# Kernel tuning notes

Hardware: AMD Instinct MI355X
Metric: run time of the kernel (lower is better)

Reference implementation:

```python
import jax, jax.numpy as jnp
import numpy as np

B, S, H, NH, HD = 4, 4096, 1024, 16, 64

def setup_inputs() -> dict:
    key = jax.random.key(0)
    ks = jax.random.split(key, 5)
    scale = 1.0 / np.sqrt(H)
    return {
        "hidden_states": jax.random.normal(ks[0], (B, S, H), dtype=jnp.float32),
        "Wq": jax.random.normal(ks[1], (H, H), dtype=jnp.float32) * scale,
        "Wk": jax.random.normal(ks[2], (H, H), dtype=jnp.float32) * scale,
        "Wv": jax.random.normal(ks[3], (H, H), dtype=jnp.float32) * scale,
        "Wo": jax.random.normal(ks[4], (H, H), dtype=jnp.float32) * scale,
    }

def reference(hidden_states, Wq, Wk, Wv, Wo):
    b, s, h = hidden_states.shape
    # torch nn.Linear: y = x @ W.T
    q = (hidden_states @ Wq.T).reshape(b, s, NH, HD)
    k = (hidden_states @ Wk.T).reshape(b, s, NH, HD)
    v = (hidden_states @ Wv.T).reshape(b, s, NH, HD)
    # feature map: ELU (as in source, no +1)
    q = jax.nn.elu(q)
    k = jax.nn.elu(k)
    # per-head kv state: sum over sequence of outer products k_s v_s^T -> [b,h,d,e]
    kv = jnp.einsum('bshd,bshe->bhde', k, v)
    out = jnp.einsum('bqhd,bhde->bqhe', q, kv)  # [b,s,h,e]
    out = out.reshape(b, s, h)
    return out @ Wo.T  # dropout p=0.0 is identity
```

## Files before the change

### kernel.cpp

```cpp
#include <hip/hip_runtime.h>
#include <cstdint>
#include <cstddef>

#define B_  4
#define S_  4096
#define H_  1024
#define NH_ 16
#define M_  (B_*S_)

typedef __bf16 bf16x8 __attribute__((ext_vector_type(8)));
typedef float  f32x4  __attribute__((ext_vector_type(4)));

__device__ __forceinline__ unsigned short f2b(float f) {
  union { float f; unsigned u; } v; v.f = f;
  unsigned r = v.u + 0x7FFFu + ((v.u >> 16) & 1u);
  return (unsigned short)(r >> 16);
}
__device__ __forceinline__ float b2f(unsigned short u) {
  union { unsigned u; float f; } v; v.u = ((unsigned)u) << 16;
  return v.f;
}

#define GLD16(g, l) __builtin_amdgcn_global_load_lds( \
    (const __attribute__((address_space(1))) void*)(g), \
    (__attribute__((address_space(3))) void*)(l), 16, 0, 0)

#define VM0()  asm volatile("s_waitcnt vmcnt(0)" ::: "memory")
#define BAR()  do { asm volatile("" ::: "memory"); __builtin_amdgcn_s_barrier(); \
                    asm volatile("" ::: "memory"); } while (0)

__global__ void cast_f32_bf16(const float* __restrict__ src,
                              unsigned short* __restrict__ dst, int n4) {
  int i = blockIdx.x * blockDim.x + threadIdx.x;
  if (i >= n4) return;
  float4 f = reinterpret_cast<const float4*>(src)[i];
  ushort4 o;
  o.x = f2b(f.x); o.y = f2b(f.y); o.z = f2b(f.z); o.w = f2b(f.w);
  reinterpret_cast<ushort4*>(dst)[i] = o;
}

__global__ void cast_w4(const float* __restrict__ w0, const float* __restrict__ w1,
                        const float* __restrict__ w2, const float* __restrict__ w3,
                        unsigned short* __restrict__ dst) {
  int i = blockIdx.x * blockDim.x + threadIdx.x;
  int w = i >> 18, j = i & 0x3FFFF;
  const float* src = (w == 0) ? w0 : (w == 1) ? w1 : (w == 2) ? w2 : w3;
  float4 f = reinterpret_cast<const float4*>(src)[j];
  ushort4 o;
  o.x = f2b(f.x); o.y = f2b(f.y); o.z = f2b(f.z); o.w = f2b(f.w);
  reinterpret_cast<ushort4*>(dst)[i] = o;
}

template<int MODE>
__global__ __launch_bounds__(512, 2) void gemm256(
    const unsigned short* __restrict__ A_,
    const unsigned short* __restrict__ Bt_,
    void* __restrict__ out) {
  __shared__ __align__(16) unsigned short LDS[2][2][16384];

  const int NTN = (MODE == 0) ? 12 : 4;
  const int nx  = gridDim.x >> 3;
  const int b2  = (blockIdx.x & 7) * nx + (blockIdx.x >> 3);
  const int tileM = (b2 / NTN) << 8;
  const int tileN = (b2 % NTN) << 8;

  const unsigned short* Bt_e =
      (MODE == 1) ? (Bt_ + ((size_t)(tileM >> 12) << 20)) : Bt_;

  const int tid  = threadIdx.x;
  const int lane = tid & 63, wv = tid >> 6;
  const int wmi  = wv >> 2;
  const int wni  = wv & 3;
  const int fr   = lane & 15, fq = lane >> 4;

  const int sr0 = tid >> 3,          sc0 = (tid & 7) ^ (sr0 & 7);
  const int sr1 = (tid + 512) >> 3,  sc1 = (tid & 7) ^ (sr1 & 7);

#define STG(NB, ARR, HM, SRC, RB, TT) do {                                      \
    GLD16((SRC) + (size_t)((RB) + (HM)*128 + sr0) * 1024 + (TT)*64 + sc0*8,     \
          &LDS[NB][ARR][(HM)*8192 + wv*512]);                                   \
    GLD16((SRC) + (size_t)((RB) + (HM)*128 + sr1) * 1024 + (TT)*64 + sc1*8,     \
          &LDS[NB][ARR][(HM)*8192 + 4096 + wv*512]);                            \
  } while (0)

#define LOADA(CB, MQ) do {                                                      \
    _Pragma("unroll")                                                           \
    for (int m = 0; m < 4; m++) {                                               \
      int r = (MQ)*128 + wmi*64 + m*16 + fr;                                    \
      af[m][0] = *(const bf16x8*)&LDS[CB][0][r*64 + ((fq    ) ^ (r&7))*8];      \
      af[m][1] = *(const bf16x8*)&LDS[CB][0][r*64 + ((4 + fq) ^ (r&7))*8];      \
    }                                                                           \
  } while (0)

#define LOADB(CB, NQ) do {                                                      \
    _Pragma("unroll")                                                           \
    for (int n = 0; n < 2; n++) {                                               \
      int r = (NQ)*128 + wni*32 + n*16 + fr;                                    \
      bv[n][0] = *(const bf16x8*)&LDS[CB][1][r*64 + ((fq    ) ^ (r&7))*8];      \
      bv[n][1] = *(const bf16x8*)&LDS[CB][1][r*64 + ((4 + fq) ^ (r&7))*8];      \
    }                                                                           \
  } while (0)

#define MM(MQ, NQ) do {                                                         \
    __builtin_amdgcn_s_setprio(1);                                              \
    _Pragma("unroll")                                                           \
    for (int m = 0; m < 4; m++)                                                 \
      _Pragma("unroll")                                                         \
      for (int n = 0; n < 2; n++) {                                             \
        acc[MQ][NQ][m][n] = __builtin_amdgcn_mfma_f32_16x16x32_bf16(            \
            af[m][0], bv[n][0], acc[MQ][NQ][m][n], 0, 0, 0);                    \
        acc[MQ][NQ][m][n] = __builtin_amdgcn_mfma_f32_16x16x32_bf16(            \
            af[m][1], bv[n][1], acc[MQ][NQ][m][n], 0, 0, 0);                    \
      }                                                                         \
    __builtin_amdgcn_s_setprio(0);                                              \
  } while (0)

  f32x4 zero = {0.f, 0.f, 0.f, 0.f};
  f32x4 acc[2][2][4][2];
#pragma unroll
  for (int a = 0; a < 2; a++)
#pragma unroll
    for (int b = 0; b < 2; b++)
#pragma unroll
      for (int m = 0; m < 4; m++)
#pragma unroll
        for (int n = 0; n < 2; n++) acc[a][b][m][n] = zero;

  bf16x8 af[4][2], bv[2][2];

  STG(0, 0, 0, A_,   tileM, 0);
  STG(0, 0, 1, A_,   tileM, 0);
  STG(0, 1, 0, Bt_e, tileN, 0);
  STG(0, 1, 1, Bt_e, tileN, 0);
  VM0();
  BAR();

  int cb = 0;
  for (int t = 0; t < 15; ++t) {
    const int nb = cb ^ 1;
    LOADA(cb, 0); LOADB(cb, 0);
    STG(nb, 0, 0, A_,   tileM, t + 1);
    STG(nb, 1, 0, Bt_e, tileN, t + 1);
    BAR(); MM(0, 0); BAR();
    LOADB(cb, 1);
    STG(nb, 1, 1, Bt_e, tileN, t + 1);
    BAR(); MM(0, 1); BAR();
    LOADA(cb, 1);
    STG(nb, 0, 1, A_,   tileM, t + 1);
    BAR(); MM(1, 1); BAR();
    LOADB(cb, 0);
    VM0();
    BAR(); MM(1, 0); BAR();
    cb = nb;
  }
  LOADA(cb, 0); LOADB(cb, 0);
  BAR(); MM(0, 0); BAR();
  LOADB(cb, 1);
  BAR(); MM(0, 1); BAR();
  LOADA(cb, 1);
  BAR(); MM(1, 1); BAR();
  LOADB(cb, 0);
  BAR(); MM(1, 0);

#pragma unroll
  for (int mq = 0; mq < 2; mq++)
#pragma unroll
    for (int nq = 0; nq < 2; nq++)
#pragma unroll
      for (int m = 0; m < 4; m++)
#pragma unroll
        for (int n = 0; n < 2; n++)
#pragma unroll
          for (int r = 0; r < 4; r++) {
            int row = tileM + mq * 128 + wmi * 64 + m * 16 + fq * 4 + r;
            int col = tileN + nq * 128 + wni * 32 + n * 16 + fr;
            float v = acc[mq][nq][m][n][r];
            if (MODE == 0) {
              int reg = col >> 10, lc = col & 1023;
              if (reg < 2) v = v > 0.f ? v : (expf(v) - 1.f);
              ((unsigned short*)out)[(size_t)reg * ((size_t)M_ * H_) +
                                     (size_t)row * H_ + lc] = f2b(v);
            } else {
              ((float*)out)[(size_t)row * H_ + col] = v;
            }
          }
#undef MM
#undef LOADB
#undef LOADA
#undef STG
}

__global__ __launch_bounds__(256) void kv_partial(
    const unsigned short* __restrict__ Kb,
    const unsigned short* __restrict__ Vb,
    float* __restrict__ kvp) {
  __shared__ __align__(16) unsigned short kt[32 * 64];
  __shared__ __align__(16) unsigned short vt[32 * 64];
  const int bh = blockIdx.x >> 4;
  const int ch = blockIdx.x & 15;
  const int b  = bh >> 4, h = bh & 15;
  const int t  = threadIdx.x;
  const int rr = t >> 3;
  const int cc = (t & 7) * 8;
  const int d0 = (t >> 4) * 4;
  const int e0 = (t & 15) * 4;

  float acc[4][4] = {};
  for (int s0 = ch * 256; s0 < ch * 256 + 256; s0 += 32) {
    size_t g = (size_t)(b * S_ + s0 + rr) * H_ + h * 64 + cc;
    *reinterpret_cast<uint4*>(&kt[rr * 64 + cc]) = *reinterpret_cast<const uint4*>(Kb + g);
    *reinterpret_cast<uint4*>(&vt[rr * 64 + cc]) = *reinterpret_cast<const uint4*>(Vb + g);
    __syncthreads();
#pragma unroll 4
    for (int ss = 0; ss < 32; ss++) {
      ushort4 k4 = *reinterpret_cast<const ushort4*>(&kt[ss * 64 + d0]);
      ushort4 v4 = *reinterpret_cast<const ushort4*>(&vt[ss * 64 + e0]);
      float kf[4] = {b2f(k4.x), b2f(k4.y), b2f(k4.z), b2f(k4.w)};
      float vf[4] = {b2f(v4.x), b2f(v4.y), b2f(v4.z), b2f(v4.w)};
#pragma unroll
      for (int i = 0; i < 4; i++)
#pragma unroll
        for (int j = 0; j < 4; j++) acc[i][j] += kf[i] * vf[j];
    }
    __syncthreads();
  }
  float* outp = kvp + (size_t)blockIdx.x * 4096;
#pragma unroll
  for (int i = 0; i < 4; i++)
#pragma unroll
    for (int j = 0; j < 4; j++) outp[(d0 + i) * 64 + e0 + j] = acc[i][j];
}

__global__ __launch_bounds__(256) void kv_reduce(
    const float* __restrict__ kvp, unsigned short* __restrict__ KVb) {
  const int bh = blockIdx.x;
#pragma unroll
  for (int i = 0; i < 16; i++) {
    int idx = threadIdx.x + i * 256;
    float s = 0.f;
#pragma unroll
    for (int ch = 0; ch < 16; ch++) s += kvp[(size_t)(bh * 16 + ch) * 4096 + idx];
    KVb[(size_t)bh * 4096 + idx] = f2b(s);
  }
}

__global__ __launch_bounds__(256) void merge_m(
    const unsigned short* __restrict__ KVb,
    const unsigned short* __restrict__ Wob,
    unsigned short* __restrict__ MbT) {
  const int bh = blockIdx.x >> 2;
  const int nc = blockIdx.x & 3;
  const int b  = bh >> 4, h = bh & 15;
  const int lane = threadIdx.x & 63, wv = threadIdx.x >> 6;
  const int fr = lane & 15, fq = lane >> 4;
  const int ncb = nc * 256 + wv * 64;

  f32x4 zero = {0.f, 0.f, 0.f, 0.f};
  f32x4 acc[4][4];
#pragma unroll
  for (int i = 0; i < 4; i++)
#pragma unroll
    for (int j = 0; j < 4; j++) acc[i][j] = zero;

#pragma unroll
  for (int kk = 0; kk < 2; kk++) {
    bf16x8 af[4], bvv[4];
#pragma unroll
    for (int i = 0; i < 4; i++)
      af[i] = *(const bf16x8*)&KVb[(size_t)bh * 4096 + (i * 16 + fr) * 64 + kk * 32 + fq * 8];
#pragma unroll
    for (int j = 0; j < 4; j++)
      bvv[j] = *(const bf16x8*)&Wob[(size_t)(ncb + j * 16 + fr) * 1024 + h * 64 + kk * 32 + fq * 8];
#pragma unroll
    for (int i = 0; i < 4; i++)
#pragma unroll
      for (int j = 0; j < 4; j++)
        acc[i][j] = __builtin_amdgcn_mfma_f32_16x16x32_bf16(af[i], bvv[j], acc[i][j], 0, 0, 0);
  }
#pragma unroll
  for (int i = 0; i < 4; i++)
#pragma unroll
    for (int j = 0; j < 4; j++)
#pragma unroll
      for (int r = 0; r < 4; r++) {
        int n = ncb + j * 16 + fr;
        int k = h * 64 + i * 16 + fq * 4 + r;
        MbT[((size_t)b << 20) + (size_t)n * 1024 + k] = f2b(acc[i][j][r]);
      }
}

extern "C" void kernel_launch(void* const* d_in, const int* in_sizes, int n_in,
                              void* d_out, int out_size, void* d_ws, size_t ws_size,
                              hipStream_t stream) {
  (void)in_sizes; (void)n_in; (void)out_size; (void)ws_size;
  const float* X  = (const float*)d_in[0];
  const float* Wq = (const float*)d_in[1];
  const float* Wk = (const float*)d_in[2];
  const float* Wv = (const float*)d_in[3];
  const float* Wo = (const float*)d_in[4];

  char*  ws  = (char*)d_ws;
  size_t off = 0;
  auto alloc = [&](size_t bytes) -> char* {
    char* p = ws + off;
    off += (bytes + 255) & ~(size_t)255;
    return p;
  };
  unsigned short* Xb   = (unsigned short*)alloc((size_t)M_ * H_ * 2);
  unsigned short* Wcat = (unsigned short*)alloc((size_t)4 * H_ * H_ * 2);
  unsigned short* QKVb = (unsigned short*)alloc((size_t)3 * M_ * H_ * 2);
  float*          kvp  = (float*)alloc((size_t)64 * 16 * 4096 * 4);
  unsigned short* KVb  = (unsigned short*)alloc((size_t)64 * 4096 * 2);
  unsigned short* MbT  = (unsigned short*)alloc((size_t)4 * H_ * H_ * 2);

  unsigned short* Qb = QKVb;
  unsigned short* Kb = QKVb + (size_t)M_ * H_;
  unsigned short* Vb = QKVb + (size_t)2 * M_ * H_;
  unsigned short* Wob = Wcat + (size_t)3 * H_ * H_;

  cast_f32_bf16<<<(M_ * H_) / 1024, 256, 0, stream>>>(X, Xb, (M_ * H_) / 4);
  cast_w4<<<(4 * H_ * H_) / 1024, 256, 0, stream>>>(Wq, Wk, Wv, Wo, Wcat);

  gemm256<0><<<768, 512, 0, stream>>>(Xb, Wcat, QKVb);

  kv_partial<<<1024, 256, 0, stream>>>(Kb, Vb, kvp);
  kv_reduce<<<64, 256, 0, stream>>>(kvp, KVb);
  merge_m<<<256, 256, 0, stream>>>(KVb, Wob, MbT);

  gemm256<1><<<256, 512, 0, stream>>>(Qb, MbT, (float*)d_out);
}
```

Baseline: 276.1 us.

## Stage GEMM epilogue through swizzled LDS for vectorized stores, hoist prefetches

The GEMM epilogue now writes accumulators into swizzled shared memory and then emits 16-byte coalesced global stores, replacing scattered 2-byte and 4-byte stores. All next-tile global-to-LDS prefetches are issued at the start of each k-iteration instead of being interleaved between MMA phases. The KV partial kernel uses 8 sequence chunks instead of 16, which halves the partial buffer and the reduce work. The costs are extra barriers and LDS traffic in the epilogue, and less parallelism in kv_partial.

```diff
diff --git a/kernel.cpp b/kernel.cpp
--- a/kernel.cpp
+++ b/kernel.cpp
@@ -140,13 +140,13 @@
     const int nb = cb ^ 1;
     LOADA(cb, 0); LOADB(cb, 0);
     STG(nb, 0, 0, A_,   tileM, t + 1);
+    STG(nb, 0, 1, A_,   tileM, t + 1);
     STG(nb, 1, 0, Bt_e, tileN, t + 1);
+    STG(nb, 1, 1, Bt_e, tileN, t + 1);
     BAR(); MM(0, 0); BAR();
     LOADB(cb, 1);
-    STG(nb, 1, 1, Bt_e, tileN, t + 1);
     BAR(); MM(0, 1); BAR();
     LOADA(cb, 1);
-    STG(nb, 0, 1, A_,   tileM, t + 1);
     BAR(); MM(1, 1); BAR();
     LOADB(cb, 0);
     VM0();
@@ -162,28 +162,64 @@
   LOADB(cb, 0);
   BAR(); MM(1, 0);
 
-#pragma unroll
-  for (int mq = 0; mq < 2; mq++)
-#pragma unroll
-    for (int nq = 0; nq < 2; nq++)
-#pragma unroll
-      for (int m = 0; m < 4; m++)
-#pragma unroll
-        for (int n = 0; n < 2; n++)
-#pragma unroll
-          for (int r = 0; r < 4; r++) {
-            int row = tileM + mq * 128 + wmi * 64 + m * 16 + fq * 4 + r;
-            int col = tileN + nq * 128 + wni * 32 + n * 16 + fr;
-            float v = acc[mq][nq][m][n][r];
-            if (MODE == 0) {
-              int reg = col >> 10, lc = col & 1023;
-              if (reg < 2) v = v > 0.f ? v : (expf(v) - 1.f);
-              ((unsigned short*)out)[(size_t)reg * ((size_t)M_ * H_) +
-                                     (size_t)row * H_ + lc] = f2b(v);
-            } else {
-              ((float*)out)[(size_t)row * H_ + col] = v;
+  if (MODE == 0) {
+    unsigned short* Ep = &LDS[0][0][0];
+    const int reg = tileN >> 10;
+    const bool doELU = (reg < 2);
+    BAR();
+#pragma unroll
+    for (int mq = 0; mq < 2; mq++)
+#pragma unroll
+      for (int nq = 0; nq < 2; nq++)
+#pragma unroll
+        for (int m = 0; m < 4; m++)
+#pragma unroll
+          for (int n = 0; n < 2; n++)
+#pragma unroll
+            for (int r = 0; r < 4; r++) {
+              int row = mq * 128 + wmi * 64 + m * 16 + fq * 4 + r;
+              int col = nq * 128 + wni * 32 + n * 16 + fr;
+              float v = acc[mq][nq][m][n][r];
+              if (doELU) v = v > 0.f ? v : (expf(v) - 1.f);
+              Ep[row * 256 + (col ^ ((row & 7) << 3))] = f2b(v);
             }
-          }
+    BAR();
+    unsigned short* outp = (unsigned short*)out + (size_t)reg * M_ * H_;
+    const int lcbase = tileN & 1023;
+#pragma unroll
+    for (int it = 0; it < 16; it++) {
+      int g = it * 512 + tid;
+      int row = g >> 5, col = (g & 31) * 8;
+      bf16x8 val = *(const bf16x8*)&Ep[row * 256 + (col ^ ((row & 7) << 3))];
+      *(bf16x8*)&outp[(size_t)(tileM + row) * H_ + lcbase + col] = val;
+    }
+  } else {
+    float* Ef = (float*)&LDS[0][0][0];
+#pragma unroll
+    for (int mq = 0; mq < 2; mq++) {
+      BAR();
+#pragma unroll
+      for (int nq = 0; nq < 2; nq++)
+#pragma unroll
+        for (int m = 0; m < 4; m++)
+#pragma unroll
+          for (int n = 0; n < 2; n++)
+#pragma unroll
+            for (int r = 0; r < 4; r++) {
+              int row = wmi * 64 + m * 16 + fq * 4 + r;
+              int col = nq * 128 + wni * 32 + n * 16 + fr;
+              Ef[row * 256 + (col ^ ((row & 7) << 2))] = acc[mq][nq][m][n][r];
+            }
+      BAR();
+#pragma unroll
+      for (int it = 0; it < 16; it++) {
+        int g = it * 512 + tid;
+        int row = g >> 6, c = (g & 63) * 4;
+        f32x4 val = *(const f32x4*)&Ef[row * 256 + (c ^ ((row & 7) << 2))];
+        *(f32x4*)&((float*)out)[(size_t)(tileM + mq * 128 + row) * H_ + tileN + c] = val;
+      }
+    }
+  }
 #undef MM
 #undef LOADB
 #undef LOADA
@@ -196,8 +232,8 @@
     float* __restrict__ kvp) {
   __shared__ __align__(16) unsigned short kt[32 * 64];
   __shared__ __align__(16) unsigned short vt[32 * 64];
-  const int bh = blockIdx.x >> 4;
-  const int ch = blockIdx.x & 15;
+  const int bh = blockIdx.x >> 3;
+  const int ch = blockIdx.x & 7;
   const int b  = bh >> 4, h = bh & 15;
   const int t  = threadIdx.x;
   const int rr = t >> 3;
@@ -206,7 +242,7 @@
   const int e0 = (t & 15) * 4;
 
   float acc[4][4] = {};
-  for (int s0 = ch * 256; s0 < ch * 256 + 256; s0 += 32) {
+  for (int s0 = ch * 512; s0 < ch * 512 + 512; s0 += 32) {
     size_t g = (size_t)(b * S_ + s0 + rr) * H_ + h * 64 + cc;
     *reinterpret_cast<uint4*>(&kt[rr * 64 + cc]) = *reinterpret_cast<const uint4*>(Kb + g);
     *reinterpret_cast<uint4*>(&vt[rr * 64 + cc]) = *reinterpret_cast<const uint4*>(Vb + g);
@@ -239,7 +275,7 @@
     int idx = threadIdx.x + i * 256;
     float s = 0.f;
 #pragma unroll
-    for (int ch = 0; ch < 16; ch++) s += kvp[(size_t)(bh * 16 + ch) * 4096 + idx];
+    for (int ch = 0; ch < 8; ch++) s += kvp[(size_t)(bh * 8 + ch) * 4096 + idx];
     KVb[(size_t)bh * 4096 + idx] = f2b(s);
   }
 }
@@ -309,7 +345,7 @@
   unsigned short* Xb   = (unsigned short*)alloc((size_t)M_ * H_ * 2);
   unsigned short* Wcat = (unsigned short*)alloc((size_t)4 * H_ * H_ * 2);
   unsigned short* QKVb = (unsigned short*)alloc((size_t)3 * M_ * H_ * 2);
-  float*          kvp  = (float*)alloc((size_t)64 * 16 * 4096 * 4);
+  float*          kvp  = (float*)alloc((size_t)64 * 8 * 4096 * 4);
   unsigned short* KVb  = (unsigned short*)alloc((size_t)64 * 4096 * 2);
   unsigned short* MbT  = (unsigned short*)alloc((size_t)4 * H_ * H_ * 2);
 
@@ -323,7 +359,7 @@
 
   gemm256<0><<<768, 512, 0, stream>>>(Xb, Wcat, QKVb);
 
-  kv_partial<<<1024, 256, 0, stream>>>(Kb, Vb, kvp);
+  kv_partial<<<512, 256, 0, stream>>>(Kb, Vb, kvp);
   kv_reduce<<<64, 256, 0, stream>>>(kvp, KVb);
   merge_m<<<256, 256, 0, stream>>>(KVb, Wob, MbT);
 
```

Measured after the change: 271.7 us. No clear change (-1.6%).
